# Kernel optimization log

Measured on AMD Instinct MI355X. Metric: run time of the kernel, lower is better.

Reference implementation:

```python
import jax, jax.numpy as jnp
import numpy as np

NTYPE = 4
NWAVE = 8
CUTOFF = 5.0
NIPSIN = np.array([0, 1, 2])
# index_para: order id repeated 3**p times -> [0, 1,1,1, 2,...(9)] length 13
INDEX_PARA = np.concatenate([np.full(3 ** int(p), i, dtype=np.int32) for i, p in enumerate(NIPSIN)])


def setup_inputs() -> dict:
    B, N, P = 8, 1000, 40000
    key = jax.random.key(0)
    ks = jax.random.split(key, 8)
    cart = jax.random.normal(ks[0], (B, N, 3), dtype=jnp.float32) * 3.0
    numatoms = jnp.full((B,), N, dtype=jnp.int32)
    species = jax.random.randint(ks[1], (B * N,), 0, NTYPE, dtype=jnp.int32)
    # neighbor list: guarantee j != i so distances are strictly positive
    i0 = jax.random.randint(ks[2], (B, P), 0, N, dtype=jnp.int32)
    off = jax.random.randint(ks[3], (B, P), 1, N, dtype=jnp.int32)
    i1 = (i0 + off) % N
    atom_index = jnp.stack([i0, i1], axis=0)  # (2, B, P)
    shifts = jnp.zeros((B, P, 3), dtype=jnp.float32)
    rs = jax.random.uniform(ks[4], (NTYPE, NWAVE), minval=0.0, maxval=CUTOFF, dtype=jnp.float32)
    inta = jax.random.uniform(ks[5], (NTYPE, NWAVE), minval=0.5, maxval=1.5, dtype=jnp.float32)
    params = jax.random.normal(ks[6], (NTYPE, len(NIPSIN) * NWAVE), dtype=jnp.float32)
    hyper = jax.random.normal(ks[7], (1, len(NIPSIN), NWAVE, NWAVE), dtype=jnp.float32)
    hyper = hyper / jnp.linalg.norm(hyper, axis=2, keepdims=True)
    return {"cart": cart, "numatoms": numatoms, "species": species,
            "atom_index": atom_index, "shifts": shifts,
            "rs": rs, "inta": inta, "params": params, "hyper": hyper}


def reference(cart, numatoms, species, atom_index, shifts, rs, inta, params, hyper):
    B, N = cart.shape[0], cart.shape[1]
    cart_ = cart.reshape(-1, 3)
    totnatom = cart_.shape[0]
    P = atom_index.shape[2]
    # offset per-molecule local indices into flat atom indices
    mol_off = (jnp.arange(B, dtype=atom_index.dtype) * N)[None, :, None]  # (1,B,1)
    idx = (atom_index + mol_off).reshape(2, -1)  # (2, E)
    sv = shifts.reshape(-1, 3)
    # gather edge endpoints
    dvec = cart_[idx[0]] - cart_[idx[1]] + sv          # (E,3)
    dist = jnp.linalg.norm(dvec, axis=-1)              # (E,)
    u = dvec / dist[:, None]                           # unit vectors
    sp = species[idx[1]]                               # (E,)
    # gaussian radial (per-species rs/inta gather instead of type loop)
    radial = jnp.exp(-inta[sp] * jnp.square(dist[:, None] - rs[sp]))   # (E,NWAVE)
    fc = jnp.square(0.5 * jnp.cos(dist * (np.pi / CUTOFF)) + 0.5)      # (E,)
    # angular: orders 0,1,2 -> rows [1; u; u (x) u] = (13, E)
    ut = u.T                                            # (3,E)
    E = ut.shape[1]
    ang = jnp.concatenate([jnp.ones((1, E), ut.dtype), ut,
                           (ut[:, None, :] * ut[None, :, :]).reshape(9, E)], axis=0)
    # fused per-edge orbital: (E, 13, NWAVE)
    orbital = jnp.einsum('je,e,ek->ejk', ang, fc, radial)
    # per-atom orbital coefficients (all species valid, mask is all-true)
    orb_coeff = params[species]                         # (T, 3*NWAVE)
    ip = jnp.asarray(INDEX_PARA)
    expandpara = hyper[0][ip]                           # (13, NWAVE, NWAVE)
    ep1 = orb_coeff[idx[1]].reshape(-1, len(NIPSIN), NWAVE)[:, ip]     # (E,13,NWAVE)
    worb = jnp.einsum('ejk,jkm,ejm->ejm', orbital, expandpara, ep1)    # (E,13,NWAVE)
    # scatter-add over center atoms
    sumw = jax.ops.segment_sum(worb, idx[0], num_segments=totnatom)    # (T,13,NWAVE)
    part_den = jnp.square(sumw)
    # index_add over angular order dim (13 -> 3)
    density = jnp.zeros((totnatom, len(NIPSIN), NWAVE), part_den.dtype).at[:, ip].add(part_den)
    return density.reshape(totnatom, -1)
```

## Files before the change

kernel.cpp:

```cpp
#include <hip/hip_runtime.h>
#include <math.h>

#define NWAVE 8
#define NTYPE 4
#define CAP   256


__global__ void __launch_bounds__(256)
fill_binned_kernel(const float* __restrict__ cart,
                   const int*   __restrict__ species,
                   const int*   __restrict__ atom_index,
                   const float* __restrict__ shifts,
                   int*         __restrict__ cursors,
                   float4*      __restrict__ payload,
                   int BP, int P, int N)
{
    int e = blockIdx.x * 256 + threadIdx.x;
    if (e >= BP) return;
    int b = e / P, base = b * N;
    int i0 = atom_index[e] + base;
    int i1 = atom_index[BP + e] + base;
    float dx = cart[3 * i0 + 0] - cart[3 * i1 + 0] + shifts[3 * e + 0];
    float dy = cart[3 * i0 + 1] - cart[3 * i1 + 1] + shifts[3 * e + 1];
    float dz = cart[3 * i0 + 2] - cart[3 * i1 + 2] + shifts[3 * e + 2];
    int sp = species[i1];
    int pos = atomicAdd(&cursors[i0], 1);
    if (pos < CAP)
        payload[(size_t)i0 * CAP + pos] = make_float4(dx, dy, dz, __int_as_float(sp));
}

__global__ void __launch_bounds__(256)
atom_gather_kernel(const float4* __restrict__ payload,
                   const int* __restrict__ cursors,
                   const float* __restrict__ rs,
                   const float* __restrict__ inta,
                   const float* __restrict__ params,
                   const float* __restrict__ hyper,
                   float* __restrict__ out, int T)
{
    __shared__ float sh_rs[NTYPE * NWAVE];
    __shared__ float sh_inta[NTYPE * NWAVE];
    int tid = threadIdx.x;
    if (tid < 32) { sh_rs[tid] = rs[tid]; sh_inta[tid] = inta[tid]; }
    __syncthreads();

    int t    = blockIdx.x * 4 + (tid >> 6);
    int lane = tid & 63;
    int s    = lane >> 3;
    int m    = lane & 7;
    if (t >= T) return;

    float hcol0[8], hcol1[8], hcol2[8];
#pragma unroll
    for (int k = 0; k < 8; ++k) {
        hcol0[k] = hyper[       k * 8 + m];
        hcol1[k] = hyper[ 64 +  k * 8 + m];
        hcol2[k] = hyper[128 +  k * 8 + m];
    }
    float par[NTYPE][3];
#pragma unroll
    for (int sp = 0; sp < NTYPE; ++sp)
#pragma unroll
        for (int p = 0; p < 3; ++p)
            par[sp][p] = params[sp * 24 + p * 8 + m];

    int cnt = cursors[t];
    if (cnt > CAP) cnt = CAP;
    const float4* __restrict__ pl = payload + (size_t)t * CAP;

    float a0 = 0.f;
    float a1x = 0.f, a1y = 0.f, a1z = 0.f;
    float axx = 0.f, ayy = 0.f, azz = 0.f, axy = 0.f, axz = 0.f, ayz = 0.f;

    for (int i = s; i < cnt; i += 8) {
        float4 d = pl[i];
        int sp = __float_as_int(d.w);
        float dx = d.x, dy = d.y, dz = d.z;
        float dist = sqrtf(dx * dx + dy * dy + dz * dz);
        float inv = 1.0f / dist;
        float ux = dx * inv, uy = dy * inv, uz = dz * inv;
        float fc = 0.5f * __cosf(dist * (float)(M_PI / 5.0)) + 0.5f;
        fc = fc * fc;
        float r0 = 0.f, r1 = 0.f, r2 = 0.f;
#pragma unroll
        for (int k = 0; k < 8; ++k) {
            float dd = dist - sh_rs[sp * 8 + k];
            float rad = __expf(-sh_inta[sp * 8 + k] * dd * dd);
            r0 += rad * hcol0[k];
            r1 += rad * hcol1[k];
            r2 += rad * hcol2[k];
        }
        float W0 = fc * r0 * par[sp][0];
        float W1 = fc * r1 * par[sp][1];
        float W2 = fc * r2 * par[sp][2];
        a0 += W0;
        a1x += ux * W1; a1y += uy * W1; a1z += uz * W1;
        float tx = ux * W2, ty = uy * W2;
        axx += tx * ux; axy += tx * uy; axz += tx * uz;
        ayy += ty * uy; ayz += ty * uz;
        azz += uz * uz * W2;
    }

#define RED(v) v += __shfl_xor(v, 8); v += __shfl_xor(v, 16); v += __shfl_xor(v, 32)
    RED(a0);
    RED(a1x); RED(a1y); RED(a1z);
    RED(axx); RED(ayy); RED(azz); RED(axy); RED(axz); RED(ayz);
#undef RED

    if (s == 0) {
        float o0 = a0 * a0;
        float o1 = a1x * a1x + a1y * a1y + a1z * a1z;
        float o2 = axx * axx + ayy * ayy + azz * azz
                 + 2.0f * (axy * axy + axz * axz + ayz * ayz);
        float* o = out + (size_t)t * 24;
        o[m] = o0; o[8 + m] = o1; o[16 + m] = o2;
    }
}

extern "C" void kernel_launch(void* const* d_in, const int* in_sizes, int n_in,
                              void* d_out, int out_size, void* d_ws, size_t ws_size,
                              hipStream_t stream)
{
    const float* cart       = (const float*)d_in[0];
    const int*   species    = (const int*)  d_in[2];
    const int*   atom_index = (const int*)  d_in[3];
    const float* shifts     = (const float*)d_in[4];
    const float* rs         = (const float*)d_in[5];
    const float* inta       = (const float*)d_in[6];
    const float* params     = (const float*)d_in[7];
    const float* hyper      = (const float*)d_in[8];

    const int B  = in_sizes[1];
    const int N  = in_sizes[2] / B;
    const int BP = in_sizes[3] / 2;
    const int P  = BP / B;
    const int T  = B * N;

    char* ws = (char*)d_ws;
    float4* payload = (float4*)ws;
    int*    cursors = (int*)(ws + (size_t)T * CAP * 16);

    hipMemsetAsync(cursors, 0, (size_t)T * sizeof(int), stream);

    fill_binned_kernel<<<(BP + 255) / 256, 256, 0, stream>>>(
        cart, species, atom_index, shifts, cursors, payload, BP, P, N);

    atom_gather_kernel<<<(T + 3) / 4, 256, 0, stream>>>(
        payload, cursors, rs, inta, params, hyper, (float*)d_out, T);
}
```

Baseline: 117.9 us.

## Fuse binning and gather into one kernel with per-chunk shared-memory accumulation

Replaces the two-pass scheme (a global atomic binning pass writing a per-atom payload, then a per-atom gather kernel) with one kernel. Each block owns 32 atoms of one molecule, scans that molecule's whole edge list to queue the edges whose center falls in its chunk, and then accumulates the angular moments with LDS atomics. This removes the memset, the global payload round-trip and a launch. In exchange every block rereads all P edge indices of its molecule, and the edge work becomes contended shared-memory atomics. The queue is capped at 2560 entries, so edges beyond that are dropped and results are wrong if a chunk has more incident edges.

```diff
diff --git a/kernel.cpp b/kernel.cpp
--- a/kernel.cpp
+++ b/kernel.cpp
@@ -3,53 +3,38 @@
 
 #define NWAVE 8
 #define NTYPE 4
-#define CAP   256
-
+#define NA    32
+#define ASTR  88
+#define QCAP  2560
 
 __global__ void __launch_bounds__(256)
-fill_binned_kernel(const float* __restrict__ cart,
-                   const int*   __restrict__ species,
-                   const int*   __restrict__ atom_index,
-                   const float* __restrict__ shifts,
-                   int*         __restrict__ cursors,
-                   float4*      __restrict__ payload,
-                   int BP, int P, int N)
+fused_density_kernel(const float* __restrict__ cart,
+                     const int*   __restrict__ species,
+                     const int*   __restrict__ atom_index,
+                     const float* __restrict__ shifts,
+                     const float* __restrict__ rs,
+                     const float* __restrict__ inta,
+                     const float* __restrict__ params,
+                     const float* __restrict__ hyper,
+                     float*       __restrict__ out,
+                     int B, int P, int N, int BP)
 {
-    int e = blockIdx.x * 256 + threadIdx.x;
-    if (e >= BP) return;
-    int b = e / P, base = b * N;
-    int i0 = atom_index[e] + base;
-    int i1 = atom_index[BP + e] + base;
-    float dx = cart[3 * i0 + 0] - cart[3 * i1 + 0] + shifts[3 * e + 0];
-    float dy = cart[3 * i0 + 1] - cart[3 * i1 + 1] + shifts[3 * e + 1];
-    float dz = cart[3 * i0 + 2] - cart[3 * i1 + 2] + shifts[3 * e + 2];
-    int sp = species[i1];
-    int pos = atomicAdd(&cursors[i0], 1);
-    if (pos < CAP)
-        payload[(size_t)i0 * CAP + pos] = make_float4(dx, dy, dz, __int_as_float(sp));
-}
-
-__global__ void __launch_bounds__(256)
-atom_gather_kernel(const float4* __restrict__ payload,
-                   const int* __restrict__ cursors,
-                   const float* __restrict__ rs,
-                   const float* __restrict__ inta,
-                   const float* __restrict__ params,
-                   const float* __restrict__ hyper,
-                   float* __restrict__ out, int T)
-{
+    __shared__ float acc[NA * ASTR];
+    __shared__ int   q[QCAP];
+    __shared__ int   q_n;
     __shared__ float sh_rs[NTYPE * NWAVE];
     __shared__ float sh_inta[NTYPE * NWAVE];
-    int tid = threadIdx.x;
+
+    const int tid = threadIdx.x;
+    const int b   = blockIdx.y;
+    const int chunk_lo = blockIdx.x * NA;
+    const int na = min(NA, N - chunk_lo);
+
+    for (int i = tid; i < NA * ASTR; i += 256) acc[i] = 0.0f;
+    if (tid == 0) q_n = 0;
     if (tid < 32) { sh_rs[tid] = rs[tid]; sh_inta[tid] = inta[tid]; }
-    __syncthreads();
 
-    int t    = blockIdx.x * 4 + (tid >> 6);
-    int lane = tid & 63;
-    int s    = lane >> 3;
-    int m    = lane & 7;
-    if (t >= T) return;
-
+    const int m = tid & 7;
     float hcol0[8], hcol1[8], hcol2[8];
 #pragma unroll
     for (int k = 0; k < 8; ++k) {
@@ -64,27 +49,45 @@
         for (int p = 0; p < 3; ++p)
             par[sp][p] = params[sp * 24 + p * 8 + m];
 
-    int cnt = cursors[t];
-    if (cnt > CAP) cnt = CAP;
-    const float4* __restrict__ pl = payload + (size_t)t * CAP;
+    __syncthreads();
 
-    float a0 = 0.f;
-    float a1x = 0.f, a1y = 0.f, a1z = 0.f;
-    float axx = 0.f, ayy = 0.f, azz = 0.f, axy = 0.f, axz = 0.f, ayz = 0.f;
+    const int*   __restrict__ ai0 = atom_index + (size_t)b * P;
+    const int*   __restrict__ ai1 = atom_index + (size_t)BP + (size_t)b * P;
+    const float* __restrict__ sh3 = shifts + (size_t)b * P * 3;
+    const int base = b * N;
 
-    for (int i = s; i < cnt; i += 8) {
-        float4 d = pl[i];
-        int sp = __float_as_int(d.w);
-        float dx = d.x, dy = d.y, dz = d.z;
+    for (int p = tid; p < P; p += 256) {
+        int a = ai0[p] - chunk_lo;
+        if ((unsigned)a < (unsigned)na) {
+            int idx = atomicAdd(&q_n, 1);
+            if (idx < QCAP) q[idx] = (a << 20) | p;
+        }
+    }
+    __syncthreads();
+    int qn = q_n; if (qn > QCAP) qn = QCAP;
+
+    for (int qi = tid >> 3; qi < qn; qi += 32) {
+        int packed = q[qi];
+        int p = packed & 0xFFFFF;
+        int a = packed >> 20;
+        int i0 = base + chunk_lo + a;
+        int i1 = ai1[p] + base;
+
+        float dx = cart[3 * i0 + 0] - cart[3 * i1 + 0] + sh3[3 * p + 0];
+        float dy = cart[3 * i0 + 1] - cart[3 * i1 + 1] + sh3[3 * p + 1];
+        float dz = cart[3 * i0 + 2] - cart[3 * i1 + 2] + sh3[3 * p + 2];
+        int sp = species[i1];
+
         float dist = sqrtf(dx * dx + dy * dy + dz * dz);
-        float inv = 1.0f / dist;
+        float inv  = 1.0f / dist;
         float ux = dx * inv, uy = dy * inv, uz = dz * inv;
         float fc = 0.5f * __cosf(dist * (float)(M_PI / 5.0)) + 0.5f;
         fc = fc * fc;
+
         float r0 = 0.f, r1 = 0.f, r2 = 0.f;
 #pragma unroll
         for (int k = 0; k < 8; ++k) {
-            float dd = dist - sh_rs[sp * 8 + k];
+            float dd  = dist - sh_rs[sp * 8 + k];
             float rad = __expf(-sh_inta[sp * 8 + k] * dd * dd);
             r0 += rad * hcol0[k];
             r1 += rad * hcol1[k];
@@ -93,26 +96,34 @@
         float W0 = fc * r0 * par[sp][0];
         float W1 = fc * r1 * par[sp][1];
         float W2 = fc * r2 * par[sp][2];
-        a0 += W0;
-        a1x += ux * W1; a1y += uy * W1; a1z += uz * W1;
+
+        float* A = acc + a * ASTR + m;
+        atomicAdd(A +  0, W0);
+        atomicAdd(A +  8, ux * W1);
+        atomicAdd(A + 16, uy * W1);
+        atomicAdd(A + 24, uz * W1);
         float tx = ux * W2, ty = uy * W2;
-        axx += tx * ux; axy += tx * uy; axz += tx * uz;
-        ayy += ty * uy; ayz += ty * uz;
-        azz += uz * uz * W2;
+        atomicAdd(A + 32, tx * ux);
+        atomicAdd(A + 40, ty * uy);
+        atomicAdd(A + 48, uz * uz * W2);
+        atomicAdd(A + 56, tx * uy);
+        atomicAdd(A + 64, tx * uz);
+        atomicAdd(A + 72, ty * uz);
     }
+    __syncthreads();
 
-#define RED(v) v += __shfl_xor(v, 8); v += __shfl_xor(v, 16); v += __shfl_xor(v, 32)
-    RED(a0);
-    RED(a1x); RED(a1y); RED(a1z);
-    RED(axx); RED(ayy); RED(azz); RED(axy); RED(axz); RED(ayz);
-#undef RED
-
-    if (s == 0) {
-        float o0 = a0 * a0;
-        float o1 = a1x * a1x + a1y * a1y + a1z * a1z;
-        float o2 = axx * axx + ayy * ayy + azz * azz
-                 + 2.0f * (axy * axy + axz * axz + ayz * ayz);
-        float* o = out + (size_t)t * 24;
+    int a = tid >> 3;
+    if (a < na) {
+        const float* A = acc + a * ASTR + m;
+        float v0 = A[0];
+        float x  = A[8],  y  = A[16], z  = A[24];
+        float xx = A[32], yy = A[40], zz = A[48];
+        float xy = A[56], xz = A[64], yz = A[72];
+        float o0 = v0 * v0;
+        float o1 = x * x + y * y + z * z;
+        float o2 = xx * xx + yy * yy + zz * zz
+                 + 2.0f * (xy * xy + xz * xz + yz * yz);
+        float* o = out + (size_t)(base + chunk_lo + a) * 24;
         o[m] = o0; o[8 + m] = o1; o[16 + m] = o2;
     }
 }
@@ -134,17 +145,10 @@
     const int N  = in_sizes[2] / B;
     const int BP = in_sizes[3] / 2;
     const int P  = BP / B;
-    const int T  = B * N;
 
-    char* ws = (char*)d_ws;
-    float4* payload = (float4*)ws;
-    int*    cursors = (int*)(ws + (size_t)T * CAP * 16);
-
-    hipMemsetAsync(cursors, 0, (size_t)T * sizeof(int), stream);
-
-    fill_binned_kernel<<<(BP + 255) / 256, 256, 0, stream>>>(
-        cart, species, atom_index, shifts, cursors, payload, BP, P, N);
-
-    atom_gather_kernel<<<(T + 3) / 4, 256, 0, stream>>>(
-        payload, cursors, rs, inta, params, hyper, (float*)d_out, T);
+    const int nchunk = (N + NA - 1) / NA;
+    dim3 grid(nchunk, B);
+    fused_density_kernel<<<grid, 256, 0, stream>>>(
+        cart, species, atom_index, shifts, rs, inta, params, hyper,
+        (float*)d_out, B, P, N, BP);
 }
```

Result: slower. 293.1 us (+148.5%).
